# Kernel tuning notes

Measured on AMD Instinct MI355X. Metric: run time of the kernel, lower is better.

## Reference

```python
import jax, jax.numpy as jnp
import numpy as np

B = 4
C = 128           # input channels
H = W = 512       # image size
P = 16            # patch size
GH = GW = 32      # token grid (H//P, W//P)
N = GH * GW       # num patches = 1024
PATCH_DIM = C * P * P  # 32768
DIM = 512         # embed dim
MLP = 256         # ffn hidden
DH = 64           # dim per head
HEADS = (2, 4, 8) # per-layer head counts
NUM_REL = (2 * GH - 1) * (2 * GW - 1)  # 3969


def _rel_index():
    # faithful to the torch buffer construction (meshgrid default 'ij')
    coords = np.stack(np.meshgrid(np.arange(GH), np.arange(GW), indexing='ij')).reshape(2, -1)
    rc = (coords[:, :, None] - coords[:, None, :]).transpose(1, 2, 0)  # [N,N,2]
    rc[..., 0] += GH - 1
    rc[..., 1] += GW - 1
    rc[..., 0] *= 2 * GH - 1
    return jnp.asarray(rc.sum(-1))  # [N,N] int

REL_IDX = _rel_index()


def _ln(x, s, b):
    m = x.mean(-1, keepdims=True)
    v = x.var(-1, keepdims=True)
    return (x - m) / jnp.sqrt(v + 1e-5) * s + b


def setup_inputs() -> dict:
    key = jax.random.key(0)
    ks = iter(jax.random.split(key, 40))
    def rn(shape, scale=0.02):
        return jax.random.normal(next(ks), shape, jnp.float32) * scale
    inp = {"img": jax.random.normal(next(ks), (B, C, H, W), jnp.float32)}
    inp["patch_w"] = rn((PATCH_DIM, DIM))
    inp["patch_b"] = jnp.zeros((DIM,), jnp.float32)
    inp["pos_emb"] = rn((1, N, DIM), 1.0)
    inp["ln1_s"] = jnp.ones((3, DIM), jnp.float32)
    inp["ln1_b"] = jnp.zeros((3, DIM), jnp.float32)
    inp["ln2_s"] = jnp.ones((3, DIM), jnp.float32)
    inp["ln2_b"] = jnp.zeros((3, DIM), jnp.float32)
    for l, h in enumerate(HEADS):
        inner = DH * h
        inp[f"qkv_w{l}"] = rn((DIM, 3 * inner))
        inp[f"out_w{l}"] = rn((inner, DIM))
        inp[f"out_b{l}"] = jnp.zeros((DIM,), jnp.float32)
        inp[f"bias{l}"] = rn((NUM_REL, h))
    inp["ff_w1"] = rn((3, DIM, MLP))
    inp["ff_b1"] = jnp.zeros((3, MLP), jnp.float32)
    inp["ff_w2"] = rn((3, MLP, DIM))
    inp["ff_b2"] = jnp.zeros((3, DIM), jnp.float32)
    return inp


def reference(img, patch_w, patch_b, pos_emb, ln1_s, ln1_b, ln2_s, ln2_b,
              qkv_w0, qkv_w1, qkv_w2, out_w0, out_w1, out_w2,
              out_b0, out_b1, out_b2, bias0, bias1, bias2,
              ff_w1, ff_b1, ff_w2, ff_b2):
    b = img.shape[0]
    # Rearrange 'b c (h p1) (w p2) -> b (h w) (p1 p2 c)'
    x = img.reshape(b, C, GH, P, GW, P).transpose(0, 2, 4, 3, 5, 1).reshape(b, N, PATCH_DIM)
    x = x @ patch_w + patch_b + pos_emb

    qkv_ws = (qkv_w0, qkv_w1, qkv_w2)
    out_ws = (out_w0, out_w1, out_w2)
    out_bs = (out_b0, out_b1, out_b2)
    tables = (bias0, bias1, bias2)

    for l, h in enumerate(HEADS):
        # attention with relative position bias
        xn = _ln(x, ln1_s[l], ln1_b[l])
        qkv = xn @ qkv_ws[l]                                  # [b, N, 3*h*DH]
        q, k, v = jnp.split(qkv, 3, axis=-1)
        q = q.reshape(b, N, h, DH).transpose(0, 2, 1, 3)      # bhnd
        k = k.reshape(b, N, h, DH).transpose(0, 2, 1, 3)
        v = v.reshape(b, N, h, DH).transpose(0, 2, 1, 3)
        dots = jnp.einsum('bhnd,bhmd->bhnm', q, k) * (DH ** -0.5)
        rel = tables[l][REL_IDX].transpose(2, 0, 1)           # [h, N, N]
        attn = jax.nn.softmax(dots + rel[None], axis=-1)
        o = jnp.einsum('bhnm,bhmd->bhnd', attn, v)
        o = o.transpose(0, 2, 1, 3).reshape(b, N, h * DH)
        x = o @ out_ws[l] + out_bs[l] + x
        # feed-forward
        xn = _ln(x, ln2_s[l], ln2_b[l])
        hmid = jax.nn.gelu(xn @ ff_w1[l] + ff_b1[l], approximate=False)
        x = hmid @ ff_w2[l] + ff_b2[l] + x

    return x.transpose(0, 2, 1).reshape(b, DIM, GH, GW)
```

## Files before the change

kernel.cpp:

```cpp
#include <hip/hip_runtime.h>

typedef unsigned short u16;
typedef __bf16 bf16x8 __attribute__((ext_vector_type(8)));
typedef float f32x4 __attribute__((ext_vector_type(4)));

#define AS1 __attribute__((address_space(1)))
#define AS3 __attribute__((address_space(3)))
#define MFMA(a,b,c) __builtin_amdgcn_mfma_f32_16x16x32_bf16(a,b,c,0,0,0)

__device__ __forceinline__ u16 f2bf(float f) {
    union { float f; unsigned u; } x; x.f = f;
    unsigned r = x.u + 0x7fffu + ((x.u >> 16) & 1u);
    return (u16)(r >> 16);
}

__global__ void k_rearrange(const float* __restrict__ img, u16* __restrict__ A,
                            int p1base, int P1C, int KC)
{
    __shared__ u16 T[128*129];
    int t = threadIdx.x;
    int bid = blockIdx.x;
    int gq = bid & 3; bid >>= 2;
    int p1loc = bid % P1C; bid /= P1C;
    int gh = bid & 31; int b = bid >> 5;
    int hrow = gh*16 + p1base + p1loc;
    const float* src = img + ((size_t)b*128*512 + hrow)*512 + gq*128;
    #pragma unroll
    for (int it = 0; it < 16; ++it) {
        int flat = it*256 + t;
        int c = flat >> 5, j4 = (flat & 31)*4;
        float4 v = *(const float4*)(src + (size_t)c*262144 + j4);
        T[c*129 + j4 + 0] = f2bf(v.x);
        T[c*129 + j4 + 1] = f2bf(v.y);
        T[c*129 + j4 + 2] = f2bf(v.z);
        T[c*129 + j4 + 3] = f2bf(v.w);
    }
    __syncthreads();
    #pragma unroll
    for (int it = 0; it < 8; ++it) {
        int flat = it*256 + t;
        int gwl = flat >> 8, rem = flat & 255;
        int p2 = rem >> 4, c0 = (rem & 15)*8;
        int j = gwl*16 + p2;
        union { u16 u[8]; uint4 v; } pk;
        #pragma unroll
        for (int i = 0; i < 8; ++i) pk.u[i] = T[(c0+i)*129 + j];
        size_t m = (size_t)b*1024 + gh*32 + gq*8 + gwl;
        *(uint4*)(A + m*KC + p1loc*2048 + p2*128 + c0) = pk.v;
    }
}

__global__ void k_transpose_cvt(const float* __restrict__ in, u16* __restrict__ o, int K, int N)
{
    __shared__ float T[32*33];
    int kt = blockIdx.x*32, nt = blockIdx.y*32;
    int t = threadIdx.x, r = t >> 5, c = t & 31;
    #pragma unroll
    for (int i = 0; i < 4; ++i)
        T[(r + i*8)*33 + c] = in[(size_t)(kt + r + i*8)*N + nt + c];
    __syncthreads();
    #pragma unroll
    for (int i = 0; i < 4; ++i)
        o[(size_t)(nt + r + i*8)*K + kt + c] = f2bf(T[c*33 + r + i*8]);
}

__global__ void k_init_x(float* __restrict__ x, const float* __restrict__ pb, const float* __restrict__ pe)
{
    int i4 = blockIdx.x*256 + threadIdx.x;
    size_t base = (size_t)i4*4;
    float4 a = *(const float4*)(pb + (base & 511));
    float4 b = *(const float4*)(pe + (base & 524287));
    float4 r = make_float4(a.x+b.x, a.y+b.y, a.z+b.z, a.w+b.w);
    *(float4*)(x + base) = r;
}

__global__ void k_ln(const float* __restrict__ x, const float* __restrict__ sc,
                     const float* __restrict__ bi, u16* __restrict__ o)
{
    int row = blockIdx.x, lane = threadIdx.x;
    const float* xr = x + (size_t)row*512 + lane*8;
    float4 v0 = *(const float4*)xr;
    float4 v1 = *(const float4*)(xr + 4);
    float vv[8] = {v0.x,v0.y,v0.z,v0.w,v1.x,v1.y,v1.z,v1.w};
    float sum = 0.f, sq = 0.f;
    #pragma unroll
    for (int i = 0; i < 8; ++i) { sum += vv[i]; sq += vv[i]*vv[i]; }
    #pragma unroll
    for (int m = 1; m < 64; m <<= 1) { sum += __shfl_xor(sum, m, 64); sq += __shfl_xor(sq, m, 64); }
    float mean = sum * (1.f/512.f);
    float var  = sq  * (1.f/512.f) - mean*mean;
    float rstd = rsqrtf(var + 1e-5f);
    int d = lane*8;
    union { u16 u[8]; uint4 v; } pk;
    #pragma unroll
    for (int i = 0; i < 8; ++i) pk.u[i] = f2bf((vv[i]-mean)*rstd*sc[d+i] + bi[d+i]);
    *(uint4*)(o + (size_t)row*512 + d) = pk.v;
}

template<int EPI>
__global__ __launch_bounds__(256) void k_gemm(
    const u16* __restrict__ A, int lda,
    const u16* __restrict__ Bt, int ldb,
    int Kblk,
    float* __restrict__ Cf, u16* __restrict__ Cb, int ldc,
    const float* __restrict__ bias)
{
    __shared__ alignas(16) u16 As[128*64];
    __shared__ alignas(16) u16 Bs[128*64];
    const int t = threadIdx.x;
    const int m0 = blockIdx.x*128, n0 = blockIdx.y*128;
    const int kz = blockIdx.z*Kblk;
    const int wave = t >> 6, lane = t & 63;
    const int wm = (wave >> 1)*64, wn = (wave & 1)*64;
    const int r16 = lane & 15, g = lane >> 4;
    const u16* Ab = A + (size_t)(m0 + (t>>3))*lda + kz + (t&7)*8;
    const u16* Bb = Bt + (size_t)(n0 + (t>>3))*ldb + kz + (t&7)*8;
    u16* Asd = As + t*8;
    u16* Bsd = Bs + t*8;
    f32x4 acc[4][4];
    const f32x4 z4 = {0.f,0.f,0.f,0.f};
    #pragma unroll
    for (int im = 0; im < 4; ++im)
        #pragma unroll
        for (int in_ = 0; in_ < 4; ++in_) acc[im][in_] = z4;

    for (int k = 0; k < Kblk; k += 64) {
        #pragma unroll
        for (int i = 0; i < 4; ++i) {
            __builtin_amdgcn_global_load_lds((AS1 void*)(Ab + (size_t)i*32*lda + k), (AS3 void*)(Asd + i*2048), 16, 0, 0);
            __builtin_amdgcn_global_load_lds((AS1 void*)(Bb + (size_t)i*32*ldb + k), (AS3 void*)(Bsd + i*2048), 16, 0, 0);
        }
        __syncthreads();
        #pragma unroll
        for (int kk = 0; kk < 64; kk += 32) {
            bf16x8 af[4], bfr[4];
            #pragma unroll
            for (int im = 0; im < 4; ++im)
                af[im] = *(const bf16x8*)(As + (wm + im*16 + r16)*64 + kk + g*8);
            #pragma unroll
            for (int in_ = 0; in_ < 4; ++in_)
                bfr[in_] = *(const bf16x8*)(Bs + (wn + in_*16 + r16)*64 + kk + g*8);
            #pragma unroll
            for (int im = 0; im < 4; ++im)
                #pragma unroll
                for (int in_ = 0; in_ < 4; ++in_)
                    acc[im][in_] = MFMA(af[im], bfr[in_], acc[im][in_]);
        }
        __syncthreads();
    }
    #pragma unroll
    for (int im = 0; im < 4; ++im) {
        int row = m0 + wm + im*16 + g*4;
        #pragma unroll
        for (int in_ = 0; in_ < 4; ++in_) {
            int col = n0 + wn + in_*16 + r16;
            #pragma unroll
            for (int r = 0; r < 4; ++r) {
                float v = acc[im][in_][r];
                size_t idx = (size_t)(row + r)*ldc + col;
                if constexpr (EPI == 0) {
                    __hip_atomic_fetch_add(&Cf[idx], v, __ATOMIC_RELAXED, __HIP_MEMORY_SCOPE_AGENT);
                } else if constexpr (EPI == 1) {
                    Cb[idx] = f2bf(v);
                } else if constexpr (EPI == 2) {
                    float xv = v + bias[col];
                    Cb[idx] = f2bf(0.5f*xv*(1.f + erff(xv*0.70710678118654752f)));
                } else {
                    Cf[idx] += v + bias[col];
                }
            }
        }
    }
}

__global__ __launch_bounds__(256) void k_attn(
    const u16* __restrict__ qkv, const float* __restrict__ bt,
    u16* __restrict__ o, int H)
{
    const int LD = 80;
    __shared__ alignas(16) u16 Qs[64*80], Ks[64*80], Vs[64*80];
    __shared__ alignas(16) u16 Ps[4][16*80];
    const int inner = H*64, s3 = 3*inner;
    const int qt = blockIdx.x, head = blockIdx.y, b = blockIdx.z;
    const int t = threadIdx.x, wave = t >> 6, lane = t & 63;
    const int r16 = lane & 15, g = lane >> 4;
    const int q0 = qt*64;
    const size_t tokbase = (size_t)b*1024;
    const int hoff = head*64;

    #pragma unroll
    for (int it = 0; it < 2; ++it) {
        int flat = it*256 + t, r = flat >> 3, d0 = (flat & 7)*8;
        uint4 v = *(const uint4*)(qkv + (tokbase + q0 + r)*s3 + hoff + d0);
        *(uint4*)(Qs + r*LD + d0) = v;
    }
    __syncthreads();
    bf16x8 aQ0 = *(const bf16x8*)(Qs + (wave*16 + r16)*LD + g*8);
    bf16x8 aQ1 = *(const bf16x8*)(Qs + (wave*16 + r16)*LD + 32 + g*8);

    float m_[4], l_[4];
    f32x4 O[4];
    const f32x4 z4 = {0.f,0.f,0.f,0.f};
    #pragma unroll
    for (int r = 0; r < 4; ++r) { m_[r] = -1e30f; l_[r] = 0.f; O[r] = z4; }
    const int qg_base = q0 + wave*16 + g*4;

    for (int kt = 0; kt < 16; ++kt) {
        const int key0 = kt*64;
        #pragma unroll
        for (int it = 0; it < 2; ++it) {
            int flat = it*256 + t, r = flat >> 3, d0 = (flat & 7)*8;
            uint4 v = *(const uint4*)(qkv + (tokbase + key0 + r)*s3 + inner + hoff + d0);
            *(uint4*)(Ks + r*LD + d0) = v;
        }
        #pragma unroll
        for (int it = 0; it < 2; ++it) {
            int flat = it*256 + t, key = flat & 63, d0 = (flat >> 6)*8;
            uint4 v = *(const uint4*)(qkv + (tokbase + key0 + key)*s3 + 2*inner + hoff + d0);
            const u16* pv = (const u16*)&v;
            #pragma unroll
            for (int i = 0; i < 8; ++i) Vs[(d0+i)*LD + key] = pv[i];
        }
        __syncthreads();

        float Sv[4][4];
        #pragma unroll
        for (int kb = 0; kb < 4; ++kb) {
            bf16x8 k0f = *(const bf16x8*)(Ks + (kb*16 + r16)*LD + g*8);
            bf16x8 k1f = *(const bf16x8*)(Ks + (kb*16 + r16)*LD + 32 + g*8);
            f32x4 S = z4;
            S = MFMA(aQ0, k0f, S);
            S = MFMA(aQ1, k1f, S);
            int keyg = key0 + kb*16 + r16;
            int kgh = keyg >> 5, kgw = keyg & 31;
            #pragma unroll
            for (int r = 0; r < 4; ++r) {
                int qg = qg_base + r;
                int rel = ((qg >> 5) - kgh + 31)*63 + ((qg & 31) - kgw + 31);
                Sv[kb][r] = S[r]*0.125f + bt[rel*H + head];
            }
        }
        float mx[4], al[4], ps[4];
        #pragma unroll
        for (int r = 0; r < 4; ++r)
            mx[r] = fmaxf(fmaxf(Sv[0][r], Sv[1][r]), fmaxf(Sv[2][r], Sv[3][r]));
        #pragma unroll
        for (int msk = 1; msk < 16; msk <<= 1)
            #pragma unroll
            for (int r = 0; r < 4; ++r) mx[r] = fmaxf(mx[r], __shfl_xor(mx[r], msk, 64));
        #pragma unroll
        for (int r = 0; r < 4; ++r) {
            float nm = fmaxf(m_[r], mx[r]);
            al[r] = __expf(m_[r] - nm);
            m_[r] = nm;
            ps[r] = 0.f;
        }
        #pragma unroll
        for (int kb = 0; kb < 4; ++kb)
            #pragma unroll
            for (int r = 0; r < 4; ++r) {
                float p = __expf(Sv[kb][r] - m_[r]);
                Sv[kb][r] = p;
                ps[r] += p;
            }
        #pragma unroll
        for (int msk = 1; msk < 16; msk <<= 1)
            #pragma unroll
            for (int r = 0; r < 4; ++r) ps[r] += __shfl_xor(ps[r], msk, 64);
        #pragma unroll
        for (int r = 0; r < 4; ++r) l_[r] = l_[r]*al[r] + ps[r];
        #pragma unroll
        for (int kb = 0; kb < 4; ++kb)
            #pragma unroll
            for (int r = 0; r < 4; ++r)
                Ps[wave][(g*4 + r)*LD + kb*16 + r16] = f2bf(Sv[kb][r]);
        #pragma unroll
        for (int dt = 0; dt < 4; ++dt)
            #pragma unroll
            for (int r = 0; r < 4; ++r) O[dt][r] = O[dt][r]*al[r];
        __syncthreads();
        bf16x8 aP0 = *(const bf16x8*)(Ps[wave] + r16*LD + g*8);
        bf16x8 aP1 = *(const bf16x8*)(Ps[wave] + r16*LD + 32 + g*8);
        #pragma unroll
        for (int dt = 0; dt < 4; ++dt) {
            bf16x8 v0 = *(const bf16x8*)(Vs + (dt*16 + r16)*LD + g*8);
            bf16x8 v1 = *(const bf16x8*)(Vs + (dt*16 + r16)*LD + 32 + g*8);
            O[dt] = MFMA(aP0, v0, O[dt]);
            O[dt] = MFMA(aP1, v1, O[dt]);
        }
        __syncthreads();
    }
    #pragma unroll
    for (int dt = 0; dt < 4; ++dt)
        #pragma unroll
        for (int r = 0; r < 4; ++r) {
            int token = q0 + wave*16 + g*4 + r;
            o[(tokbase + token)*inner + hoff + dt*16 + r16] = f2bf(O[dt][r] / l_[r]);
        }
}

__global__ void k_out_transpose(const float* __restrict__ x, float* __restrict__ o)
{
    __shared__ float T[32*33];
    int d0 = blockIdx.x*32, n0 = blockIdx.y*32, b = blockIdx.z;
    int t = threadIdx.x, r = t >> 5, c = t & 31;
    #pragma unroll
    for (int i = 0; i < 4; ++i)
        T[(r+i*8)*33 + c] = x[((size_t)b*1024 + n0 + r + i*8)*512 + d0 + c];
    __syncthreads();
    #pragma unroll
    for (int i = 0; i < 4; ++i)
        o[((size_t)b*512 + d0 + r + i*8)*1024 + n0 + c] = T[c*33 + (r+i*8)];
}

extern "C" void kernel_launch(void* const* d_in, const int* in_sizes, int n_in,
                              void* d_out, int out_size, void* d_ws, size_t ws_size,
                              hipStream_t stream)
{
    (void)in_sizes; (void)n_in; (void)out_size;
    const float* img     = (const float*)d_in[0];
    const float* patch_w = (const float*)d_in[1];
    const float* patch_b = (const float*)d_in[2];
    const float* pos_emb = (const float*)d_in[3];
    const float* ln1_s   = (const float*)d_in[4];
    const float* ln1_b   = (const float*)d_in[5];
    const float* ln2_s   = (const float*)d_in[6];
    const float* ln2_b   = (const float*)d_in[7];
    const float* qkv_w[3] = {(const float*)d_in[8],  (const float*)d_in[12], (const float*)d_in[16]};
    const float* out_w[3] = {(const float*)d_in[9],  (const float*)d_in[13], (const float*)d_in[17]};
    const float* out_b[3] = {(const float*)d_in[10], (const float*)d_in[14], (const float*)d_in[18]};
    const float* biasT[3] = {(const float*)d_in[11], (const float*)d_in[15], (const float*)d_in[19]};
    const float* ff_w1 = (const float*)d_in[20];
    const float* ff_b1 = (const float*)d_in[21];
    const float* ff_w2 = (const float*)d_in[22];
    const float* ff_b2 = (const float*)d_in[23];
    float* out = (float*)d_out;

    char* ws = (char*)d_ws;
    size_t off = 0;
    auto alloc = [&](size_t bytes) -> void* {
        void* p = ws + off; off += (bytes + 255) & ~(size_t)255; return p;
    };
    u16*   pwT  = (u16*)  alloc(512ull*32768*2);
    float* x    = (float*)alloc(4096ull*512*4);
    u16*   xn   = (u16*)  alloc(4096ull*512*2);
    u16*   qkv  = (u16*)  alloc(4096ull*1536*2);
    u16*   ob   = (u16*)  alloc(4096ull*512*2);
    u16*   mid  = (u16*)  alloc(4096ull*256*2);
    u16*   qkvT = (u16*)  alloc(1536ull*512*2);
    u16*   outT = (u16*)  alloc(512ull*512*2);
    u16*   f1T  = (u16*)  alloc(256ull*512*2);
    u16*   f2T  = (u16*)  alloc(512ull*256*2);
    size_t fixed = off;
    bool full = (ws_size >= fixed + 4096ull*32768*2 + 4096);
    int P1C = full ? 16 : 4;
    int NCH = full ? 1 : 4;
    int SPL = full ? 8 : 4;
    int KC  = P1C*2048;
    u16* A = (u16*)alloc((size_t)4096*KC*2);

    k_transpose_cvt<<<dim3(1024,16), 256, 0, stream>>>(patch_w, pwT, 32768, 512);
    k_init_x<<<2048, 256, 0, stream>>>(x, patch_b, pos_emb);
    for (int c = 0; c < NCH; ++c) {
        k_rearrange<<<4*32*P1C*4, 256, 0, stream>>>(img, A, c*P1C, P1C, KC);
        k_gemm<0><<<dim3(32,4,SPL), 256, 0, stream>>>(A, KC, pwT + (size_t)c*P1C*2048, 32768,
                                                      KC/SPL, x, nullptr, 512, nullptr);
    }

    const int HS[3] = {2,4,8};
    for (int l = 0; l < 3; ++l) {
        int h = HS[l], inner = 64*h, n3 = 3*inner;
        k_transpose_cvt<<<dim3(16, n3/32),    256, 0, stream>>>(qkv_w[l], qkvT, 512, n3);
        k_transpose_cvt<<<dim3(inner/32, 16), 256, 0, stream>>>(out_w[l], outT, inner, 512);
        k_transpose_cvt<<<dim3(16, 8),        256, 0, stream>>>(ff_w1 + (size_t)l*512*256, f1T, 512, 256);
        k_transpose_cvt<<<dim3(8, 16),        256, 0, stream>>>(ff_w2 + (size_t)l*256*512, f2T, 256, 512);

        k_ln<<<4096, 64, 0, stream>>>(x, ln1_s + l*512, ln1_b + l*512, xn);
        k_gemm<1><<<dim3(32, n3/128), 256, 0, stream>>>(xn, 512, qkvT, 512, 512,
                                                        nullptr, qkv, n3, nullptr);
        k_attn<<<dim3(16, h, 4), 256, 0, stream>>>(qkv, biasT[l], ob, h);
        k_gemm<3><<<dim3(32, 4), 256, 0, stream>>>(ob, inner, outT, inner, inner,
                                                   x, nullptr, 512, out_b[l]);
        k_ln<<<4096, 64, 0, stream>>>(x, ln2_s + l*512, ln2_b + l*512, xn);
        k_gemm<2><<<dim3(32, 2), 256, 0, stream>>>(xn, 512, f1T, 512, 512,
                                                   nullptr, mid, 256, ff_b1 + l*256);
        k_gemm<3><<<dim3(32, 4), 256, 0, stream>>>(mid, 256, f2T, 256, 256,
                                                   x, nullptr, 512, ff_b2 + l*512);
    }
    k_out_transpose<<<dim3(16, 32, 4), 256, 0, stream>>>(x, out);
}
```

Before: 879.0 us.

## Fuse image rearrange into patch-embedding GEMM with weight permuted to channel-last order

Removes the separate rearrange kernel and its bf16 staging buffer. The image is instead loaded straight from fp32, converted and written into swizzled LDS tiles inside a new 1024-thread patch GEMM. The patch weight is transposed with a permuted K ordering so each K chunk matches a contiguous image row span. The new GEMM double-buffers A and B in LDS, loads B with global_load_lds, and uses an 8-way K split with atomic accumulation. This avoids writing and rereading a 256MB intermediate, at the cost of a large-LDS, low-occupancy kernel.

```diff
diff --git a/kernel.cpp b/kernel.cpp
--- a/kernel.cpp
+++ b/kernel.cpp
@@ -14,54 +14,28 @@
     return (u16)(r >> 16);
 }
 
-__global__ void k_rearrange(const float* __restrict__ img, u16* __restrict__ A,
-                            int p1base, int P1C, int KC)
-{
-    __shared__ u16 T[128*129];
+__global__ void k_patch_wT(const float* __restrict__ w, u16* __restrict__ o)
+{
+    __shared__ u16 T[256*33];
+    int c = blockIdx.x, n0 = blockIdx.y*32;
     int t = threadIdx.x;
-    int bid = blockIdx.x;
-    int gq = bid & 3; bid >>= 2;
-    int p1loc = bid % P1C; bid /= P1C;
-    int gh = bid & 31; int b = bid >> 5;
-    int hrow = gh*16 + p1base + p1loc;
-    const float* src = img + ((size_t)b*128*512 + hrow)*512 + gq*128;
-    #pragma unroll
-    for (int it = 0; it < 16; ++it) {
-        int flat = it*256 + t;
-        int c = flat >> 5, j4 = (flat & 31)*4;
-        float4 v = *(const float4*)(src + (size_t)c*262144 + j4);
-        T[c*129 + j4 + 0] = f2bf(v.x);
-        T[c*129 + j4 + 1] = f2bf(v.y);
-        T[c*129 + j4 + 2] = f2bf(v.z);
-        T[c*129 + j4 + 3] = f2bf(v.w);
+    int rr = t >> 5, cc = t & 31;
+    #pragma unroll
+    for (int i = 0; i < 32; ++i) {
+        int r = i*8 + rr;
+        int k = (r >> 4)*2048 + (r & 15)*128 + c;
+        T[r*33 + cc] = f2bf(w[(size_t)k*512 + n0 + cc]);
     }
     __syncthreads();
     #pragma unroll
-    for (int it = 0; it < 8; ++it) {
-        int flat = it*256 + t;
-        int gwl = flat >> 8, rem = flat & 255;
-        int p2 = rem >> 4, c0 = (rem & 15)*8;
-        int j = gwl*16 + p2;
+    for (int i = 0; i < 4; ++i) {
+        int j  = i*8 + (t >> 5);
+        int ch = t & 31;
         union { u16 u[8]; uint4 v; } pk;
         #pragma unroll
-        for (int i = 0; i < 8; ++i) pk.u[i] = T[(c0+i)*129 + j];
-        size_t m = (size_t)b*1024 + gh*32 + gq*8 + gwl;
-        *(uint4*)(A + m*KC + p1loc*2048 + p2*128 + c0) = pk.v;
-    }
-}
-
-__global__ void k_transpose_cvt(const float* __restrict__ in, u16* __restrict__ o, int K, int N)
-{
-    __shared__ float T[32*33];
-    int kt = blockIdx.x*32, nt = blockIdx.y*32;
-    int t = threadIdx.x, r = t >> 5, c = t & 31;
-    #pragma unroll
-    for (int i = 0; i < 4; ++i)
-        T[(r + i*8)*33 + c] = in[(size_t)(kt + r + i*8)*N + nt + c];
-    __syncthreads();
-    #pragma unroll
-    for (int i = 0; i < 4; ++i)
-        o[(size_t)(nt + r + i*8)*K + kt + c] = f2bf(T[c*33 + r + i*8]);
+        for (int q = 0; q < 8; ++q) pk.u[q] = T[(ch*8+q)*33 + j];
+        *(uint4*)(o + (size_t)(n0 + j)*32768 + c*256 + ch*8) = pk.v;
+    }
 }
 
 __global__ void k_init_x(float* __restrict__ x, const float* __restrict__ pb, const float* __restrict__ pe)
@@ -72,6 +46,116 @@
     float4 b = *(const float4*)(pe + (base & 524287));
     float4 r = make_float4(a.x+b.x, a.y+b.y, a.z+b.z, a.w+b.w);
     *(float4*)(x + base) = r;
+}
+
+__global__ __launch_bounds__(1024) void k_patch_gemm(
+    const float* __restrict__ img, const u16* __restrict__ Bt, float* __restrict__ Cf)
+{
+    __shared__ alignas(16) u16 As[2*128*64];
+    __shared__ alignas(16) u16 Bs[2*512*64];
+    const int t = threadIdx.x;
+    const int bid = blockIdx.x;
+    const int z = bid & 7;
+    const int tile = bid >> 3;
+    const int b = tile >> 3, gh0 = (tile & 7)*4;
+    const int m0 = tile*128;
+    const int wave = t >> 6, lane = t & 63;
+    const int r16 = lane & 15, g = lane >> 4;
+    const int wm = (wave >> 3)*64, wn = (wave & 7)*64;
+
+    const int arow = t >> 6;
+    const int ghl = arow >> 2, p1l = arow & 3;
+    const int aw = (t & 63)*8;
+    const int tok = ghl*32 + (aw >> 4);
+    unsigned abyte = (unsigned)(tok*128 + p1l*32 + (aw & 15)*2);
+    abyte ^= (unsigned)((tok & 7) << 4);
+    const float* imgb = img + (size_t)b*128*262144
+                      + (size_t)((gh0 + ghl)*16 + p1l)*512 + aw;
+    const int brow = t >> 3;
+    const int bchunk = (t & 7) ^ (brow & 7);
+    const u16* Bb = Bt + (size_t)brow*32768 + (size_t)z*4096 + bchunk*8;
+    u16* Bsd = Bs + t*8;
+
+    f32x4 acc[4][4];
+    const f32x4 zz = {0.f,0.f,0.f,0.f};
+    #pragma unroll
+    for (int im = 0; im < 4; ++im)
+        #pragma unroll
+        for (int in_ = 0; in_ < 4; ++in_) acc[im][in_] = zz;
+
+#define STAGE(KC, BUF) do {                                                          \
+    const int c_ = z*16 + ((KC) >> 2);                                               \
+    const float* src_ = imgb + (size_t)c_*262144 + ((KC) & 3)*2048;                  \
+    float4 a0_ = *(const float4*)src_;                                               \
+    float4 a1_ = *(const float4*)(src_ + 4);                                         \
+    _Pragma("unroll")                                                                \
+    for (int i_ = 0; i_ < 4; ++i_)                                                   \
+        __builtin_amdgcn_global_load_lds((AS1 void*)(Bb + (size_t)i_*128*32768 + (KC)*64), \
+                                         (AS3 void*)(Bsd + (BUF)*32768 + i_*8192), 16, 0, 0); \
+    union { u16 u[8]; uint4 v; } pk_;                                                \
+    pk_.u[0]=f2bf(a0_.x); pk_.u[1]=f2bf(a0_.y); pk_.u[2]=f2bf(a0_.z); pk_.u[3]=f2bf(a0_.w); \
+    pk_.u[4]=f2bf(a1_.x); pk_.u[5]=f2bf(a1_.y); pk_.u[6]=f2bf(a1_.z); pk_.u[7]=f2bf(a1_.w); \
+    *(uint4*)((char*)As + (BUF)*16384 + abyte) = pk_.v;                              \
+} while(0)
+
+    STAGE(0, 0);
+    __syncthreads();
+    int cur = 0;
+    for (int kc = 0; kc < 64; ++kc) {
+        if (kc < 63) STAGE(kc + 1, cur ^ 1);
+        const char* Asb = (const char*)As + cur*16384;
+        const char* Bsb = (const char*)Bs + cur*65536;
+        #pragma unroll
+        for (int kk = 0; kk < 64; kk += 32) {
+            bf16x8 af[4], bfr[4];
+            #pragma unroll
+            for (int im = 0; im < 4; ++im) {
+                unsigned off = ((unsigned)((wm + im*16 + r16)*128 + kk*2 + g*16))
+                             ^ (unsigned)((r16 & 7) << 4);
+                af[im] = *(const bf16x8*)(Asb + off);
+            }
+            #pragma unroll
+            for (int in_ = 0; in_ < 4; ++in_) {
+                unsigned off = ((unsigned)((wn + in_*16 + r16)*128 + kk*2 + g*16))
+                             ^ (unsigned)((r16 & 7) << 4);
+                bfr[in_] = *(const bf16x8*)(Bsb + off);
+            }
+            #pragma unroll
+            for (int im = 0; im < 4; ++im)
+                #pragma unroll
+                for (int in_ = 0; in_ < 4; ++in_)
+                    acc[im][in_] = MFMA(af[im], bfr[in_], acc[im][in_]);
+        }
+        __syncthreads();
+        cur ^= 1;
+    }
+#undef STAGE
+    #pragma unroll
+    for (int im = 0; im < 4; ++im) {
+        int row = m0 + wm + im*16 + g*4;
+        #pragma unroll
+        for (int in_ = 0; in_ < 4; ++in_) {
+            int col = wn + in_*16 + r16;
+            #pragma unroll
+            for (int r = 0; r < 4; ++r)
+                __hip_atomic_fetch_add(&Cf[(size_t)(row + r)*512 + col], acc[im][in_][r],
+                                       __ATOMIC_RELAXED, __HIP_MEMORY_SCOPE_AGENT);
+        }
+    }
+}
+
+__global__ void k_transpose_cvt(const float* __restrict__ in, u16* __restrict__ o, int K, int N)
+{
+    __shared__ float T[32*33];
+    int kt = blockIdx.x*32, nt = blockIdx.y*32;
+    int t = threadIdx.x, r = t >> 5, c = t & 31;
+    #pragma unroll
+    for (int i = 0; i < 4; ++i)
+        T[(r + i*8)*33 + c] = in[(size_t)(kt + r + i*8)*N + nt + c];
+    __syncthreads();
+    #pragma unroll
+    for (int i = 0; i < 4; ++i)
+        o[(size_t)(nt + r + i*8)*K + kt + c] = f2bf(T[c*33 + r + i*8]);
 }
 
 __global__ void k_ln(const float* __restrict__ x, const float* __restrict__ sc,
@@ -158,9 +242,7 @@
             for (int r = 0; r < 4; ++r) {
                 float v = acc[im][in_][r];
                 size_t idx = (size_t)(row + r)*ldc + col;
-                if constexpr (EPI == 0) {
-                    __hip_atomic_fetch_add(&Cf[idx], v, __ATOMIC_RELAXED, __HIP_MEMORY_SCOPE_AGENT);
-                } else if constexpr (EPI == 1) {
+                if constexpr (EPI == 1) {
                     Cb[idx] = f2bf(v);
                 } else if constexpr (EPI == 2) {
                     float xv = v + bias[col];
@@ -317,7 +399,7 @@
                               void* d_out, int out_size, void* d_ws, size_t ws_size,
                               hipStream_t stream)
 {
-    (void)in_sizes; (void)n_in; (void)out_size;
+    (void)in_sizes; (void)n_in; (void)out_size; (void)ws_size;
     const float* img     = (const float*)d_in[0];
     const float* patch_w = (const float*)d_in[1];
     const float* patch_b = (const float*)d_in[2];
@@ -351,21 +433,10 @@
     u16*   outT = (u16*)  alloc(512ull*512*2);
     u16*   f1T  = (u16*)  alloc(256ull*512*2);
     u16*   f2T  = (u16*)  alloc(512ull*256*2);
-    size_t fixed = off;
-    bool full = (ws_size >= fixed + 4096ull*32768*2 + 4096);
-    int P1C = full ? 16 : 4;
-    int NCH = full ? 1 : 4;
-    int SPL = full ? 8 : 4;
-    int KC  = P1C*2048;
-    u16* A = (u16*)alloc((size_t)4096*KC*2);
-
-    k_transpose_cvt<<<dim3(1024,16), 256, 0, stream>>>(patch_w, pwT, 32768, 512);
+
+    k_patch_wT<<<dim3(128,16), 256, 0, stream>>>(patch_w, pwT);
     k_init_x<<<2048, 256, 0, stream>>>(x, patch_b, pos_emb);
-    for (int c = 0; c < NCH; ++c) {
-        k_rearrange<<<4*32*P1C*4, 256, 0, stream>>>(img, A, c*P1C, P1C, KC);
-        k_gemm<0><<<dim3(32,4,SPL), 256, 0, stream>>>(A, KC, pwT + (size_t)c*P1C*2048, 32768,
-                                                      KC/SPL, x, nullptr, 512, nullptr);
-    }
+    k_patch_gemm<<<256, 1024, 0, stream>>>(img, pwT, x);
 
     const int HS[3] = {2,4,8};
     for (int l = 0; l < 3; ++l) {
```

After: 707.6 us. -19.5%, faster.
